# Performance work log

Hardware: AMD Instinct MI355X
Metric: run time of the kernel (lower is better)

Reference implementation:

```python
import jax, jax.numpy as jnp
import numpy as np

NEG_FILL = -1000.0

def setup_inputs() -> dict:
    key = jax.random.key(0)
    k1, k2, k3, k4 = jax.random.split(key, 4)
    B, N, D = 16, 2048, 64
    q = jax.random.normal(k1, (B, N, D), dtype=jnp.float32)
    k = jax.random.normal(k2, (B, N, D), dtype=jnp.float32)
    v = jax.random.normal(k3, (B, N, D), dtype=jnp.float32)
    mask = jax.random.randint(k4, (B, N, N), 0, 2) == 1
    return {"q": q, "k": k, "v": v, "mask": mask}

def reference(q, k, v, mask):
    # Faithful to the torch module: scale by sqrt(seq_len) = len(q[0])**0.5,
    # masked positions set to -1000.0, softmax over dim=1 (NOT the last dim).
    seq_len = q.shape[1]
    scores = jnp.einsum('bnd,bmd->bnm', q, k) / jnp.sqrt(jnp.float32(seq_len))
    scores = jnp.where(mask, NEG_FILL, scores)
    attn = jax.nn.softmax(scores, axis=1)  # dim=1 as in nn.Softmax(dim=1)
    out = jnp.einsum('bnm,bmd->bnd', attn, v)
    return out
```

## Files before the change

### kernel.cpp

```cpp
#include <hip/hip_runtime.h>
#include <hip/hip_bf16.h>


#define B_ 16
#define N_ 2048
#define D_ 64
#define SCALE 0.022097086912079608f
#define NWORD (N_ / 32)

typedef __attribute__((ext_vector_type(8))) short bf16x8;
typedef __attribute__((ext_vector_type(4))) float f32x4;

static __device__ __forceinline__ short f2bf(float x) {
  unsigned u = __float_as_uint(x);
  return (short)((u + 0x7FFF + ((u >> 16) & 1)) >> 16);
}

static __device__ __forceinline__ bf16x8 load8(const short* p) {
  return *reinterpret_cast<const bf16x8*>(p);
}

static __device__ __forceinline__ bf16x8 load8f(const float* p) {
  const f32x4 a = *reinterpret_cast<const f32x4*>(p);
  const f32x4 b = *reinterpret_cast<const f32x4*>(p + 4);
  bf16x8 r;
  r[0] = f2bf(a[0]); r[1] = f2bf(a[1]); r[2] = f2bf(a[2]); r[3] = f2bf(a[3]);
  r[4] = f2bf(b[0]); r[5] = f2bf(b[1]); r[6] = f2bf(b[2]); r[7] = f2bf(b[3]);
  return r;
}

__global__ __launch_bounds__(256) void pack_mask(const int* __restrict__ mask,
                                                 unsigned* __restrict__ bits) {
  const size_t w = (size_t)blockIdx.x * 256 + threadIdx.x;
  const int4* p = reinterpret_cast<const int4*>(mask) + w * 8;
  unsigned r = 0;
#pragma unroll
  for (int j = 0; j < 8; ++j) {
    const int4 x = p[j];
    r |= (x.x ? 1u : 0u) << (j * 4);
    r |= (x.y ? 1u : 0u) << (j * 4 + 1);
    r |= (x.z ? 1u : 0u) << (j * 4 + 2);
    r |= (x.w ? 1u : 0u) << (j * 4 + 3);
  }
  bits[w] = r;
}

__global__ __launch_bounds__(256) void cvt_bf16(const float* __restrict__ q,
                                                const float* __restrict__ k,
                                                short* __restrict__ qb,
                                                short* __restrict__ kb) {
  const size_t i = ((size_t)blockIdx.x * 256 + threadIdx.x) * 8;
  const float* src = blockIdx.y ? k : q;
  short* dst = blockIdx.y ? kb : qb;
  *reinterpret_cast<bf16x8*>(dst + i) = load8f(src + i);
}

__global__ __launch_bounds__(256) void colsum_kernel(
    const short* __restrict__ qb, const short* __restrict__ kb,
    const unsigned* __restrict__ bits, float* __restrict__ colsum) {
  const int b = blockIdx.x;
  const int wave = threadIdx.x >> 6;
  const int lane = threadIdx.x & 63;
  const int l15 = lane & 15;
  const int lhi = lane >> 4;
  const int m0 = blockIdx.y * 128 + wave * 32;
  const int wword = m0 >> 5;

  const short* qbb = qb + (size_t)b * N_ * D_;
  const short* kbb = kb + (size_t)b * N_ * D_;
  const unsigned* bitsb = bits + (size_t)b * N_ * NWORD;

  bf16x8 kf[2][2];
#pragma unroll
  for (int cg = 0; cg < 2; ++cg) {
    kf[cg][0] = load8(kbb + (m0 + cg * 16 + l15) * D_ + lhi * 8);
    kf[cg][1] = load8(kbb + (m0 + cg * 16 + l15) * D_ + 32 + lhi * 8);
  }

  float part[2] = {0.f, 0.f};
  for (int n0 = 0; n0 < N_; n0 += 16) {
    const bf16x8 qf0 = load8(qbb + (n0 + l15) * D_ + lhi * 8);
    const bf16x8 qf1 = load8(qbb + (n0 + l15) * D_ + 32 + lhi * 8);
    unsigned w[4];
#pragma unroll
    for (int r = 0; r < 4; ++r) w[r] = bitsb[(n0 + lhi * 4 + r) * NWORD + wword];
#pragma unroll
    for (int cg = 0; cg < 2; ++cg) {
      f32x4 acc = {0.f, 0.f, 0.f, 0.f};
      acc = __builtin_amdgcn_mfma_f32_16x16x32_bf16(qf0, kf[cg][0], acc, 0, 0, 0);
      acc = __builtin_amdgcn_mfma_f32_16x16x32_bf16(qf1, kf[cg][1], acc, 0, 0, 0);
#pragma unroll
      for (int r = 0; r < 4; ++r) {
        const unsigned msk = (w[r] >> (cg * 16 + l15)) & 1u;
        part[cg] += msk ? 0.f : __expf(acc[r] * SCALE);
      }
    }
  }
#pragma unroll
  for (int cg = 0; cg < 2; ++cg) {
    float p = part[cg];
    p += __shfl_xor(p, 16, 64);
    p += __shfl_xor(p, 32, 64);
    if (lane < 16) colsum[(size_t)b * N_ + m0 + cg * 16 + l15] = p;
  }
}

__global__ __launch_bounds__(256) void vprep_kernel(
    const float* __restrict__ v, const float* __restrict__ colsum,
    short* __restrict__ vt) {
  const int b = blockIdx.x;
  const int m0 = blockIdx.y * 64;
  const int tid = threadIdx.x;
  __shared__ float lds[64][65];

  const float* vb = v + (size_t)b * N_ * D_;
  const float* csb = colsum + (size_t)b * N_;
#pragma unroll
  for (int pass = 0; pass < 4; ++pass) {
    const int mloc = pass * 16 + (tid >> 4);
    const int d4 = (tid & 15) * 4;
    const f32x4 x = *reinterpret_cast<const f32x4*>(vb + (m0 + mloc) * D_ + d4);
    const float ic = 1.0f / csb[m0 + mloc];
    lds[mloc][d4 + 0] = x[0] * ic;
    lds[mloc][d4 + 1] = x[1] * ic;
    lds[mloc][d4 + 2] = x[2] * ic;
    lds[mloc][d4 + 3] = x[3] * ic;
  }
  __syncthreads();
  const int d = tid >> 2;
  const int seg = tid & 3;
  bf16x8 o0, o1;
#pragma unroll
  for (int i = 0; i < 8; ++i) o0[i] = f2bf(lds[seg * 16 + i][d]);
#pragma unroll
  for (int i = 0; i < 8; ++i) o1[i] = f2bf(lds[seg * 16 + 8 + i][d]);
  short* dst = vt + (size_t)b * D_ * N_ + (size_t)d * N_ + m0 + seg * 16;
  *reinterpret_cast<bf16x8*>(dst) = o0;
  *reinterpret_cast<bf16x8*>(dst + 8) = o1;
}

__global__ __launch_bounds__(256) void attn_out_kernel(
    const short* __restrict__ qb, const short* __restrict__ kb,
    const short* __restrict__ vt, const unsigned* __restrict__ bits,
    float* __restrict__ out) {
  const int b = blockIdx.x;
  const int wave = threadIdx.x >> 6;
  const int lane = threadIdx.x & 63;
  const int l15 = lane & 15;
  const int lhi = lane >> 4;
  const int n0 = blockIdx.y * 64 + wave * 16;

  const short* qbb = qb + (size_t)b * N_ * D_;
  const short* kbb = kb + (size_t)b * N_ * D_;
  const short* vtb = vt + (size_t)b * D_ * N_;
  const unsigned* bitsb = bits + (size_t)b * N_ * NWORD;

  const bf16x8 qf0 = load8(qbb + (n0 + l15) * D_ + lhi * 8);
  const bf16x8 qf1 = load8(qbb + (n0 + l15) * D_ + 32 + lhi * 8);

  __shared__ __align__(16) short pbuf[4][16][32];

  f32x4 oacc[4];
#pragma unroll
  for (int d = 0; d < 4; ++d) oacc[d] = (f32x4){0.f, 0.f, 0.f, 0.f};

  for (int m0 = 0; m0 < N_; m0 += 32) {
    unsigned w[4];
#pragma unroll
    for (int r = 0; r < 4; ++r)
      w[r] = bitsb[(n0 + lhi * 4 + r) * NWORD + (m0 >> 5)];
#pragma unroll
    for (int cg = 0; cg < 2; ++cg) {
      const int mc = m0 + cg * 16;
      const bf16x8 kf0 = load8(kbb + (mc + l15) * D_ + lhi * 8);
      const bf16x8 kf1 = load8(kbb + (mc + l15) * D_ + 32 + lhi * 8);
      f32x4 acc = {0.f, 0.f, 0.f, 0.f};
      acc = __builtin_amdgcn_mfma_f32_16x16x32_bf16(qf0, kf0, acc, 0, 0, 0);
      acc = __builtin_amdgcn_mfma_f32_16x16x32_bf16(qf1, kf1, acc, 0, 0, 0);
#pragma unroll
      for (int r = 0; r < 4; ++r) {
        const unsigned msk = (w[r] >> (cg * 16 + l15)) & 1u;
        const float p = msk ? 0.f : __expf(acc[r] * SCALE);
        pbuf[wave][lhi * 4 + r][cg * 16 + l15] = f2bf(p);
      }
    }
    __builtin_amdgcn_wave_barrier();
    asm volatile("s_waitcnt lgkmcnt(0)" ::: "memory");
    const bf16x8 pa =
        *reinterpret_cast<const bf16x8*>(&pbuf[wave][l15][lhi * 8]);
#pragma unroll
    for (int dsub = 0; dsub < 4; ++dsub) {
      const bf16x8 vf =
          load8(vtb + (size_t)(dsub * 16 + l15) * N_ + m0 + lhi * 8);
      oacc[dsub] =
          __builtin_amdgcn_mfma_f32_16x16x32_bf16(pa, vf, oacc[dsub], 0, 0, 0);
    }
    __builtin_amdgcn_wave_barrier();
    asm volatile("" ::: "memory");
  }

#pragma unroll
  for (int dsub = 0; dsub < 4; ++dsub)
#pragma unroll
    for (int r = 0; r < 4; ++r)
      out[(size_t)b * N_ * D_ + (size_t)(n0 + lhi * 4 + r) * D_ + dsub * 16 +
          l15] = oacc[dsub][r];
}

__global__ __launch_bounds__(256) void colsum_fb(
    const float* __restrict__ q, const float* __restrict__ k,
    const int* __restrict__ mask, float* __restrict__ colsum) {
  const int b = blockIdx.x;
  const int wave = threadIdx.x >> 6;
  const int lane = threadIdx.x & 63;
  const int l15 = lane & 15;
  const int lhi = lane >> 4;
  const int m0 = blockIdx.y * 64 + wave * 16;
  const float* qbp = q + (size_t)b * N_ * D_;
  const float* kbp = k + (size_t)b * N_ * D_;
  const int* maskb = mask + (size_t)b * N_ * N_;
  const bf16x8 kf0 = load8f(kbp + (m0 + l15) * D_ + lhi * 8);
  const bf16x8 kf1 = load8f(kbp + (m0 + l15) * D_ + 32 + lhi * 8);
  float partial = 0.f;
  for (int n0 = 0; n0 < N_; n0 += 16) {
    bf16x8 qf0 = load8f(qbp + (n0 + l15) * D_ + lhi * 8);
    bf16x8 qf1 = load8f(qbp + (n0 + l15) * D_ + 32 + lhi * 8);
    f32x4 acc = {0.f, 0.f, 0.f, 0.f};
    acc = __builtin_amdgcn_mfma_f32_16x16x32_bf16(qf0, kf0, acc, 0, 0, 0);
    acc = __builtin_amdgcn_mfma_f32_16x16x32_bf16(qf1, kf1, acc, 0, 0, 0);
#pragma unroll
    for (int r = 0; r < 4; ++r) {
      const int n = n0 + lhi * 4 + r;
      partial += maskb[(size_t)n * N_ + m0 + l15] ? 0.f
                                                  : __expf(acc[r] * SCALE);
    }
  }
  partial += __shfl_xor(partial, 16, 64);
  partial += __shfl_xor(partial, 32, 64);
  if (lane < 16) colsum[(size_t)b * N_ + m0 + l15] = partial;
}

__global__ __launch_bounds__(256) void attn_out_fb(
    const float* __restrict__ q, const float* __restrict__ k,
    const float* __restrict__ v, const int* __restrict__ mask,
    const float* __restrict__ colsum, float* __restrict__ out) {
  const int b = blockIdx.x;
  const int wave = threadIdx.x >> 6;
  const int lane = threadIdx.x & 63;
  const int l15 = lane & 15;
  const int lhi = lane >> 4;
  const int n0 = blockIdx.y * 64 + wave * 16;
  const float* qbp = q + (size_t)b * N_ * D_;
  const float* kbp = k + (size_t)b * N_ * D_;
  const float* vbp = v + (size_t)b * N_ * D_;
  const int* maskb = mask + (size_t)b * N_ * N_;
  const float* csb = colsum + (size_t)b * N_;
  const bf16x8 qf0 = load8f(qbp + (n0 + l15) * D_ + lhi * 8);
  const bf16x8 qf1 = load8f(qbp + (n0 + l15) * D_ + 32 + lhi * 8);
  __shared__ __align__(16) short pbuf[4][16][32];
  f32x4 oacc[4];
#pragma unroll
  for (int d = 0; d < 4; ++d) oacc[d] = (f32x4){0.f, 0.f, 0.f, 0.f};
  for (int m0 = 0; m0 < N_; m0 += 32) {
#pragma unroll
    for (int cg = 0; cg < 2; ++cg) {
      const int mc = m0 + cg * 16;
      bf16x8 kf0 = load8f(kbp + (mc + l15) * D_ + lhi * 8);
      bf16x8 kf1 = load8f(kbp + (mc + l15) * D_ + 32 + lhi * 8);
      f32x4 acc = {0.f, 0.f, 0.f, 0.f};
      acc = __builtin_amdgcn_mfma_f32_16x16x32_bf16(qf0, kf0, acc, 0, 0, 0);
      acc = __builtin_amdgcn_mfma_f32_16x16x32_bf16(qf1, kf1, acc, 0, 0, 0);
      const float ic = 1.0f / csb[mc + l15];
#pragma unroll
      for (int r = 0; r < 4; ++r) {
        const int n = n0 + lhi * 4 + r;
        const float p = maskb[(size_t)n * N_ + mc + l15]
                            ? 0.f
                            : __expf(acc[r] * SCALE) * ic;
        pbuf[wave][lhi * 4 + r][cg * 16 + l15] = f2bf(p);
      }
    }
    __syncthreads();
    const bf16x8 pa =
        *reinterpret_cast<const bf16x8*>(&pbuf[wave][l15][lhi * 8]);
#pragma unroll
    for (int dsub = 0; dsub < 4; ++dsub) {
      bf16x8 vf;
#pragma unroll
      for (int j = 0; j < 8; ++j)
        vf[j] = f2bf(vbp[(m0 + lhi * 8 + j) * D_ + dsub * 16 + l15]);
      oacc[dsub] =
          __builtin_amdgcn_mfma_f32_16x16x32_bf16(pa, vf, oacc[dsub], 0, 0, 0);
    }
    __syncthreads();
  }
#pragma unroll
  for (int dsub = 0; dsub < 4; ++dsub)
#pragma unroll
    for (int r = 0; r < 4; ++r)
      out[(size_t)b * N_ * D_ + (size_t)(n0 + lhi * 4 + r) * D_ + dsub * 16 +
          l15] = oacc[dsub][r];
}

extern "C" void kernel_launch(void* const* d_in, const int* in_sizes, int n_in,
                              void* d_out, int out_size, void* d_ws,
                              size_t ws_size, hipStream_t stream) {
  const float* q = (const float*)d_in[0];
  const float* k = (const float*)d_in[1];
  const float* v = (const float*)d_in[2];
  const int* mask = (const int*)d_in[3];
  float* out = (float*)d_out;

  const size_t cs_off = 0;
  const size_t qb_off = 128 * 1024;
  const size_t kb_off = qb_off + 4 * 1024 * 1024;
  const size_t vt_off = kb_off + 4 * 1024 * 1024;
  const size_t bt_off = vt_off + 4 * 1024 * 1024;
  const size_t need = bt_off + 8 * 1024 * 1024;

  float* colsum = (float*)((char*)d_ws + cs_off);

  if (ws_size >= need) {
    short* qbf = (short*)((char*)d_ws + qb_off);
    short* kbf = (short*)((char*)d_ws + kb_off);
    short* vt = (short*)((char*)d_ws + vt_off);
    unsigned* bits = (unsigned*)((char*)d_ws + bt_off);

    pack_mask<<<(B_ * N_ * NWORD) / 256, 256, 0, stream>>>(mask, bits);
    cvt_bf16<<<dim3((B_ * N_ * D_) / (256 * 8), 2), 256, 0, stream>>>(
        q, k, qbf, kbf);
    colsum_kernel<<<dim3(B_, N_ / 128), 256, 0, stream>>>(qbf, kbf, bits,
                                                          colsum);
    vprep_kernel<<<dim3(B_, N_ / 64), 256, 0, stream>>>(v, colsum, vt);
    attn_out_kernel<<<dim3(B_, N_ / 64), 256, 0, stream>>>(qbf, kbf, vt, bits,
                                                           out);
  } else {
    colsum_fb<<<dim3(B_, N_ / 64), 256, 0, stream>>>(q, k, mask, colsum);
    attn_out_fb<<<dim3(B_, N_ / 64), 256, 0, stream>>>(q, k, v, mask, colsum,
                                                       out);
  }
}
```

Measured before the change: 557.3 us.

## Split colsum and attention-output reductions across grid z for more parallelism

Splits the reduction dimension of both colsum_kernel and attn_out_kernel into four chunks using a third grid dimension. Each chunk writes partial sums to workspace. vprep sums the colsum partials, and a new reduce_out kernel adds the four output partials. The aim is to raise block count, since the original grids had only 256 or 512 blocks, and so improve occupancy across CUs. In exchange it adds extra workspace traffic of about 32 MB of partial writes and reads, plus one more kernel launch.

```diff
diff --git a/kernel.cpp b/kernel.cpp
--- a/kernel.cpp
+++ b/kernel.cpp
@@ -7,6 +7,8 @@
 #define D_ 64
 #define SCALE 0.022097086912079608f
 #define NWORD (N_ / 32)
+#define MCH 4
+#define NCH 4
 
 typedef __attribute__((ext_vector_type(8))) short bf16x8;
 typedef __attribute__((ext_vector_type(4))) float f32x4;
@@ -57,7 +59,7 @@
 
 __global__ __launch_bounds__(256) void colsum_kernel(
     const short* __restrict__ qb, const short* __restrict__ kb,
-    const unsigned* __restrict__ bits, float* __restrict__ colsum) {
+    const unsigned* __restrict__ bits, float* __restrict__ csp) {
   const int b = blockIdx.x;
   const int wave = threadIdx.x >> 6;
   const int lane = threadIdx.x & 63;
@@ -65,6 +67,7 @@
   const int lhi = lane >> 4;
   const int m0 = blockIdx.y * 128 + wave * 32;
   const int wword = m0 >> 5;
+  const int nbase = blockIdx.z * (N_ / NCH);
 
   const short* qbb = qb + (size_t)b * N_ * D_;
   const short* kbb = kb + (size_t)b * N_ * D_;
@@ -78,12 +81,13 @@
   }
 
   float part[2] = {0.f, 0.f};
-  for (int n0 = 0; n0 < N_; n0 += 16) {
+  for (int n0 = nbase; n0 < nbase + N_ / NCH; n0 += 16) {
     const bf16x8 qf0 = load8(qbb + (n0 + l15) * D_ + lhi * 8);
     const bf16x8 qf1 = load8(qbb + (n0 + l15) * D_ + 32 + lhi * 8);
     unsigned w[4];
 #pragma unroll
-    for (int r = 0; r < 4; ++r) w[r] = bitsb[(n0 + lhi * 4 + r) * NWORD + wword];
+    for (int r = 0; r < 4; ++r)
+      w[r] = bitsb[(n0 + lhi * 4 + r) * NWORD + wword];
 #pragma unroll
     for (int cg = 0; cg < 2; ++cg) {
       f32x4 acc = {0.f, 0.f, 0.f, 0.f};
@@ -101,12 +105,14 @@
     float p = part[cg];
     p += __shfl_xor(p, 16, 64);
     p += __shfl_xor(p, 32, 64);
-    if (lane < 16) colsum[(size_t)b * N_ + m0 + cg * 16 + l15] = p;
+    if (lane < 16)
+      csp[(size_t)blockIdx.z * B_ * N_ + (size_t)b * N_ + m0 + cg * 16 + l15] =
+          p;
   }
 }
 
 __global__ __launch_bounds__(256) void vprep_kernel(
-    const float* __restrict__ v, const float* __restrict__ colsum,
+    const float* __restrict__ v, const float* __restrict__ csp,
     short* __restrict__ vt) {
   const int b = blockIdx.x;
   const int m0 = blockIdx.y * 64;
@@ -114,13 +120,16 @@
   __shared__ float lds[64][65];
 
   const float* vb = v + (size_t)b * N_ * D_;
-  const float* csb = colsum + (size_t)b * N_;
 #pragma unroll
   for (int pass = 0; pass < 4; ++pass) {
     const int mloc = pass * 16 + (tid >> 4);
     const int d4 = (tid & 15) * 4;
     const f32x4 x = *reinterpret_cast<const f32x4*>(vb + (m0 + mloc) * D_ + d4);
-    const float ic = 1.0f / csb[m0 + mloc];
+    float cs = 0.f;
+#pragma unroll
+    for (int z = 0; z < NCH; ++z)
+      cs += csp[(size_t)z * B_ * N_ + (size_t)b * N_ + m0 + mloc];
+    const float ic = 1.0f / cs;
     lds[mloc][d4 + 0] = x[0] * ic;
     lds[mloc][d4 + 1] = x[1] * ic;
     lds[mloc][d4 + 2] = x[2] * ic;
@@ -142,13 +151,14 @@
 __global__ __launch_bounds__(256) void attn_out_kernel(
     const short* __restrict__ qb, const short* __restrict__ kb,
     const short* __restrict__ vt, const unsigned* __restrict__ bits,
-    float* __restrict__ out) {
+    float* __restrict__ outp) {
   const int b = blockIdx.x;
   const int wave = threadIdx.x >> 6;
   const int lane = threadIdx.x & 63;
   const int l15 = lane & 15;
   const int lhi = lane >> 4;
   const int n0 = blockIdx.y * 64 + wave * 16;
+  const int mbase = blockIdx.z * (N_ / MCH);
 
   const short* qbb = qb + (size_t)b * N_ * D_;
   const short* kbb = kb + (size_t)b * N_ * D_;
@@ -164,7 +174,7 @@
 #pragma unroll
   for (int d = 0; d < 4; ++d) oacc[d] = (f32x4){0.f, 0.f, 0.f, 0.f};
 
-  for (int m0 = 0; m0 < N_; m0 += 32) {
+  for (int m0 = mbase; m0 < mbase + N_ / MCH; m0 += 32) {
     unsigned w[4];
 #pragma unroll
     for (int r = 0; r < 4; ++r)
@@ -196,15 +206,27 @@
           __builtin_amdgcn_mfma_f32_16x16x32_bf16(pa, vf, oacc[dsub], 0, 0, 0);
     }
     __builtin_amdgcn_wave_barrier();
-    asm volatile("" ::: "memory");
-  }
-
+  }
+
+  float* dst = outp + (size_t)blockIdx.z * B_ * N_ * D_ + (size_t)b * N_ * D_;
 #pragma unroll
   for (int dsub = 0; dsub < 4; ++dsub)
 #pragma unroll
     for (int r = 0; r < 4; ++r)
-      out[(size_t)b * N_ * D_ + (size_t)(n0 + lhi * 4 + r) * D_ + dsub * 16 +
-          l15] = oacc[dsub][r];
+      dst[(size_t)(n0 + lhi * 4 + r) * D_ + dsub * 16 + l15] = oacc[dsub][r];
+}
+
+__global__ __launch_bounds__(256) void reduce_out(const float* __restrict__ outp,
+                                                  float* __restrict__ out) {
+  const size_t i = ((size_t)blockIdx.x * 256 + threadIdx.x) * 4;
+  f32x4 s = *reinterpret_cast<const f32x4*>(outp + i);
+#pragma unroll
+  for (int z = 1; z < MCH; ++z) {
+    const f32x4 x =
+        *reinterpret_cast<const f32x4*>(outp + (size_t)z * B_ * N_ * D_ + i);
+    s[0] += x[0]; s[1] += x[1]; s[2] += x[2]; s[3] += x[3];
+  }
+  *reinterpret_cast<f32x4*>(out + i) = s;
 }
 
 __global__ __launch_bounds__(256) void colsum_fb(
@@ -231,8 +253,8 @@
 #pragma unroll
     for (int r = 0; r < 4; ++r) {
       const int n = n0 + lhi * 4 + r;
-      partial += maskb[(size_t)n * N_ + m0 + l15] ? 0.f
-                                                  : __expf(acc[r] * SCALE);
+      partial +=
+          maskb[(size_t)n * N_ + m0 + l15] ? 0.f : __expf(acc[r] * SCALE);
     }
   }
   partial += __shfl_xor(partial, 16, 64);
@@ -311,30 +333,34 @@
   const int* mask = (const int*)d_in[3];
   float* out = (float*)d_out;
 
+  const size_t MB = 1024 * 1024;
   const size_t cs_off = 0;
-  const size_t qb_off = 128 * 1024;
-  const size_t kb_off = qb_off + 4 * 1024 * 1024;
-  const size_t vt_off = kb_off + 4 * 1024 * 1024;
-  const size_t bt_off = vt_off + 4 * 1024 * 1024;
-  const size_t need = bt_off + 8 * 1024 * 1024;
-
-  float* colsum = (float*)((char*)d_ws + cs_off);
+  const size_t qb_off = cs_off + NCH * (size_t)B_ * N_ * 4;
+  const size_t kb_off = qb_off + 4 * MB;
+  const size_t vt_off = kb_off + 4 * MB;
+  const size_t bt_off = vt_off + 4 * MB;
+  const size_t op_off = bt_off + 8 * MB;
+  const size_t need = op_off + (size_t)MCH * B_ * N_ * D_ * 4;
 
   if (ws_size >= need) {
+    float* csp = (float*)((char*)d_ws + cs_off);
     short* qbf = (short*)((char*)d_ws + qb_off);
     short* kbf = (short*)((char*)d_ws + kb_off);
     short* vt = (short*)((char*)d_ws + vt_off);
     unsigned* bits = (unsigned*)((char*)d_ws + bt_off);
+    float* outp = (float*)((char*)d_ws + op_off);
 
     pack_mask<<<(B_ * N_ * NWORD) / 256, 256, 0, stream>>>(mask, bits);
     cvt_bf16<<<dim3((B_ * N_ * D_) / (256 * 8), 2), 256, 0, stream>>>(
         q, k, qbf, kbf);
-    colsum_kernel<<<dim3(B_, N_ / 128), 256, 0, stream>>>(qbf, kbf, bits,
-                                                          colsum);
-    vprep_kernel<<<dim3(B_, N_ / 64), 256, 0, stream>>>(v, colsum, vt);
-    attn_out_kernel<<<dim3(B_, N_ / 64), 256, 0, stream>>>(qbf, kbf, vt, bits,
-                                                           out);
+    colsum_kernel<<<dim3(B_, N_ / 128, NCH), 256, 0, stream>>>(qbf, kbf, bits,
+                                                               csp);
+    vprep_kernel<<<dim3(B_, N_ / 64), 256, 0, stream>>>(v, csp, vt);
+    attn_out_kernel<<<dim3(B_, N_ / 64, MCH), 256, 0, stream>>>(qbf, kbf, vt,
+                                                                bits, outp);
+    reduce_out<<<(B_ * N_ * D_) / (256 * 4), 256, 0, stream>>>(outp, out);
   } else {
+    float* colsum = (float*)d_ws;
     colsum_fb<<<dim3(B_, N_ / 64), 256, 0, stream>>>(q, k, mask, colsum);
     attn_out_fb<<<dim3(B_, N_ / 64), 256, 0, stream>>>(q, k, v, mask, colsum,
                                                        out);
```

Result: faster. 542.4 us (-2.7%).
